# Kernel optimization log

Hardware: AMD Instinct MI355X
Metric: run time of the kernel (lower is better)

The kernel has to match this reference:

```python
import jax, jax.numpy as jnp
import numpy as np

SLOPE = 0.1
HEADS = 4
BN_EPS = 1e-5


def _gat(x, W, a_src, a_dst, mask):
    # x: (B,N,D); W: (D,D); a_src/a_dst: (H,dh); mask: (B,N,N) bool
    B, N, D = x.shape
    dh = D // HEADS
    h = (x @ W).reshape(B, N, HEADS, dh)
    s_src = jnp.einsum('bnhd,hd->bhn', h, a_src)  # score contrib of query i
    s_dst = jnp.einsum('bnhd,hd->bhn', h, a_dst)  # score contrib of key j
    e = jax.nn.leaky_relu(s_src[:, :, :, None] + s_dst[:, :, None, :], SLOPE)  # (B,H,N,N)
    e = jnp.where(mask[:, None, :, :], e, jnp.float32(-1e9))
    a = jax.nn.softmax(e, axis=-1)
    out = jnp.einsum('bhij,bjhd->bihd', a, h).reshape(B, N, D)
    return out


def setup_inputs() -> dict:
    key = jax.random.key(0)
    ks = jax.random.split(key, 20)
    B, N, F, D, Hn = 2, 2000, 64, 128, 3
    deep_dim = 3 * D
    feats = jax.random.normal(ks[0], (B, N, F), dtype=jnp.float32)
    ind = jax.random.randint(ks[1], (B, N, N), 0, 2).astype(bool)
    eye = jnp.eye(N, dtype=bool)[None]
    ind = jnp.logical_or(ind, eye)  # ensure self-loops so no all-masked row
    uni = jnp.ones((B, N, N), dtype=bool)
    s = 0.05
    return {
        'features': feats,
        'industry_mask': ind,
        'universe_mask': uni,
        # BatchNorm1d (eval mode)
        'bn_gamma': jax.random.normal(ks[2], (F,)) * s + 1.0,
        'bn_beta': jax.random.normal(ks[3], (F,)) * s,
        'bn_mean': jnp.zeros((F,), jnp.float32),
        'bn_var': jnp.ones((F,), jnp.float32),
        # encoder MLP (stored as (in,out))
        'W1': jax.random.normal(ks[4], (F, D)) * s,
        'b1': jnp.zeros((D,), jnp.float32),
        'W2': jax.random.normal(ks[5], (D, D)) * s,
        'b2': jnp.zeros((D,), jnp.float32),
        # industry GAT
        'giW': jax.random.normal(ks[6], (D, D)) * s,
        'gia_src': jax.random.normal(ks[7], (HEADS, D // HEADS)) * s,
        'gia_dst': jax.random.normal(ks[8], (HEADS, D // HEADS)) * s,
        # universe GAT
        'guW': jax.random.normal(ks[9], (D, D)) * s,
        'gua_src': jax.random.normal(ks[10], (HEADS, D // HEADS)) * s,
        'gua_dst': jax.random.normal(ks[11], (HEADS, D // HEADS)) * s,
        # per-horizon deep factor heads (Hn, deep_dim), (Hn,)
        'head_W': jax.random.normal(ks[12], (Hn, deep_dim)) * s,
        'head_b': jnp.zeros((Hn,), jnp.float32),
        # per-horizon factor attention proj (Hn, F, F), applied as x @ P_h^T
        'proj_W': jax.random.normal(ks[13], (Hn, F, F)) * s,
    }


def reference(features, industry_mask, universe_mask, bn_gamma, bn_beta, bn_mean,
              bn_var, W1, b1, W2, b2, giW, gia_src, gia_dst, guW, gua_src,
              gua_dst, head_W, head_b, proj_W):
    # --- StockContextEncoder: BN (eval) + MLP ---
    xn = (features - bn_mean) * jax.lax.rsqrt(bn_var + BN_EPS) * bn_gamma + bn_beta
    C = jax.nn.relu(xn @ W1 + b1) @ W2 + b2  # (B,N,D)
    # --- masked GATs with residual subtraction ---
    H_I = _gat(C, giW, gia_src, gia_dst, industry_mask)
    C_bar_I = C - H_I
    H_U = _gat(C_bar_I, guW, gua_src, gua_dst, universe_mask)
    C_bar_U = C_bar_I - H_U
    concat_ctx = jnp.concatenate([C, C_bar_I, C_bar_U], axis=-1)  # (B,N,3D)
    # --- per-horizon deep factor heads (vectorized over horizons) ---
    factors = jax.nn.leaky_relu(
        jnp.einsum('bnd,hd->hbn', concat_ctx, head_W) + head_b[:, None, None], SLOPE)
    # --- FactorAttention (Eq. 9-12), vectorized over horizons ---
    U = jax.nn.leaky_relu(jnp.einsum('bnm,hkm->hbnk', features, proj_W), SLOPE)
    A = jax.nn.softmax(U, axis=-1)          # (Hn,B,N,m)
    a_bar = A.mean(axis=2)                  # (Hn,B,m)
    recon = jnp.einsum('bnm,hbm->hbn', features, a_bar)
    return (C, C_bar_I, C_bar_U, H_I, H_U, factors, recon, A)
```

## Files before the change

kernel.cpp:

```cpp
#include <hip/hip_runtime.h>

#define BB 2
#define NN 2000
#define FF 64
#define DD 128
#define NH 4
#define HNZ 3
#define DEEP 384
#define NSEG 4
#define SEGSTRIDE 512
#define HTPAD 2048
#define SEGTOT (BB * NN * DD)
#define DENTOT (BB * NN * NH)

typedef __attribute__((ext_vector_type(8))) short short8;
typedef __attribute__((ext_vector_type(4))) float f32x4;
typedef unsigned short ushort_t;
typedef unsigned int uint_t;

__device__ __forceinline__ float lrelu(float x) { return x > 0.f ? x : 0.1f * x; }
__device__ __forceinline__ ushort_t f2bf(float f) {
    unsigned int u = __float_as_uint(f);
    unsigned int r = u + 0x7fffu + ((u >> 16) & 1u);
    return (ushort_t)(r >> 16);
}

__device__ __forceinline__ void proj_scores(
    const float (*Xl)[DD], const float* __restrict__ Wg,
    const float* __restrict__ a_src, const float* __restrict__ a_dst,
    ushort_t* __restrict__ hT, float* __restrict__ ssrc,
    float* __restrict__ sdst, int row0, int t)
{
    const int jq = t & 31, rg = t >> 5;
    const int r0 = 2 * rg, c0 = 4 * jq;
    float4 p0 = make_float4(0.f, 0.f, 0.f, 0.f);
    float4 p1 = make_float4(0.f, 0.f, 0.f, 0.f);
    for (int k = 0; k < DD; ++k) {
        float4 w = *(const float4*)&Wg[k * DD + c0];
        float x0 = Xl[r0][k], x1 = Xl[r0 + 1][k];
        p0.x += x0 * w.x; p0.y += x0 * w.y; p0.z += x0 * w.z; p0.w += x0 * w.w;
        p1.x += x1 * w.x; p1.y += x1 * w.y; p1.z += x1 * w.z; p1.w += x1 * w.w;
    }
    const int gr = row0 + r0;
    const int b = gr / NN, n = gr % NN;
    uint_t pk;
    pk = (uint_t)f2bf(p0.x) | ((uint_t)f2bf(p1.x) << 16);
    *(uint_t*)&hT[(b * DD + c0 + 0) * HTPAD + n] = pk;
    pk = (uint_t)f2bf(p0.y) | ((uint_t)f2bf(p1.y) << 16);
    *(uint_t*)&hT[(b * DD + c0 + 1) * HTPAD + n] = pk;
    pk = (uint_t)f2bf(p0.z) | ((uint_t)f2bf(p1.z) << 16);
    *(uint_t*)&hT[(b * DD + c0 + 2) * HTPAD + n] = pk;
    pk = (uint_t)f2bf(p0.w) | ((uint_t)f2bf(p1.w) << 16);
    *(uint_t*)&hT[(b * DD + c0 + 3) * HTPAD + n] = pk;

    float4 as4 = *(const float4*)&a_src[c0];
    float4 ad4 = *(const float4*)&a_dst[c0];
    float ps0 = p0.x * as4.x + p0.y * as4.y + p0.z * as4.z + p0.w * as4.w;
    float ps1 = p1.x * as4.x + p1.y * as4.y + p1.z * as4.z + p1.w * as4.w;
    float pd0 = p0.x * ad4.x + p0.y * ad4.y + p0.z * ad4.z + p0.w * ad4.w;
    float pd1 = p1.x * ad4.x + p1.y * ad4.y + p1.z * ad4.z + p1.w * ad4.w;
#pragma unroll
    for (int off = 1; off <= 4; off <<= 1) {
        ps0 += __shfl_xor(ps0, off);
        ps1 += __shfl_xor(ps1, off);
        pd0 += __shfl_xor(pd0, off);
        pd1 += __shfl_xor(pd1, off);
    }
    if ((jq & 7) == 0) {
        int h = jq >> 3;
        ssrc[(b * NH + h) * NN + n] = ps0;
        ssrc[(b * NH + h) * NN + n + 1] = ps1;
        sdst[(b * NH + h) * NN + n] = pd0;
        sdst[(b * NH + h) * NN + n + 1] = pd1;
    }
}

__global__ __launch_bounds__(256) void k_enc_proj(
    const float* __restrict__ feat, const float* __restrict__ gamma,
    const float* __restrict__ beta, const float* __restrict__ mean,
    const float* __restrict__ var, const float* __restrict__ W1,
    const float* __restrict__ b1, const float* __restrict__ W2,
    const float* __restrict__ b2, float* __restrict__ C,
    const float* __restrict__ Wg, const float* __restrict__ a_src,
    const float* __restrict__ a_dst, ushort_t* __restrict__ hT,
    float* __restrict__ ssrc, float* __restrict__ sdst)
{
    __shared__ float xnl[16][FF];
    __shared__ float hidl[16][DD];
    __shared__ float Cl[16][DD];
    const int row0 = blockIdx.x * 16;
    const int t = threadIdx.x;
    {
        int row = t >> 4, m0 = (t & 15) * 4;
        float4 f = *(const float4*)&feat[(row0 + row) * FF + m0];
        float4 g4 = *(const float4*)&gamma[m0];
        float4 be4 = *(const float4*)&beta[m0];
        float4 mn4 = *(const float4*)&mean[m0];
        float4 vr4 = *(const float4*)&var[m0];
        float4 xv;
        xv.x = (f.x - mn4.x) * rsqrtf(vr4.x + 1e-5f) * g4.x + be4.x;
        xv.y = (f.y - mn4.y) * rsqrtf(vr4.y + 1e-5f) * g4.y + be4.y;
        xv.z = (f.z - mn4.z) * rsqrtf(vr4.z + 1e-5f) * g4.z + be4.z;
        xv.w = (f.w - mn4.w) * rsqrtf(vr4.w + 1e-5f) * g4.w + be4.w;
        *(float4*)&xnl[row][m0] = xv;
    }
    __syncthreads();
    const int jq = t & 31, rg = t >> 5;
    const int r0 = 2 * rg, c0 = 4 * jq;
    float4 bb = *(const float4*)&b1[c0];
    float4 a0 = bb, a1 = bb;
    for (int k = 0; k < FF; ++k) {
        float4 w = *(const float4*)&W1[k * DD + c0];
        float x0 = xnl[r0][k], x1 = xnl[r0 + 1][k];
        a0.x += x0 * w.x; a0.y += x0 * w.y; a0.z += x0 * w.z; a0.w += x0 * w.w;
        a1.x += x1 * w.x; a1.y += x1 * w.y; a1.z += x1 * w.z; a1.w += x1 * w.w;
    }
    a0.x = fmaxf(a0.x, 0.f); a0.y = fmaxf(a0.y, 0.f);
    a0.z = fmaxf(a0.z, 0.f); a0.w = fmaxf(a0.w, 0.f);
    a1.x = fmaxf(a1.x, 0.f); a1.y = fmaxf(a1.y, 0.f);
    a1.z = fmaxf(a1.z, 0.f); a1.w = fmaxf(a1.w, 0.f);
    *(float4*)&hidl[r0][c0] = a0;
    *(float4*)&hidl[r0 + 1][c0] = a1;
    __syncthreads();
    bb = *(const float4*)&b2[c0];
    a0 = bb; a1 = bb;
    for (int k = 0; k < DD; ++k) {
        float4 w = *(const float4*)&W2[k * DD + c0];
        float x0 = hidl[r0][k], x1 = hidl[r0 + 1][k];
        a0.x += x0 * w.x; a0.y += x0 * w.y; a0.z += x0 * w.z; a0.w += x0 * w.w;
        a1.x += x1 * w.x; a1.y += x1 * w.y; a1.z += x1 * w.z; a1.w += x1 * w.w;
    }
    *(float4*)&C[(row0 + r0) * DD + c0] = a0;
    *(float4*)&C[(row0 + r0 + 1) * DD + c0] = a1;
    *(float4*)&Cl[r0][c0] = a0;
    *(float4*)&Cl[r0 + 1][c0] = a1;
    __syncthreads();
    proj_scores(Cl, Wg, a_src, a_dst, hT, ssrc, sdst, row0, t);
}

__global__ __launch_bounds__(256) void k_finish_proj(
    const float* __restrict__ C, const float* __restrict__ num_p,
    const float* __restrict__ den_p, float* __restrict__ H,
    float* __restrict__ Cbar, const float* __restrict__ Wg,
    const float* __restrict__ a_src, const float* __restrict__ a_dst,
    ushort_t* __restrict__ hT, float* __restrict__ ssrc,
    float* __restrict__ sdst)
{
    __shared__ float Xl[16][DD];
    __shared__ float denl[16][NH];
    const int row0 = blockIdx.x * 16;
    const int t = threadIdx.x;
    if (t < 64) {
        int rr = t >> 2, hh = t & 3;
        int gr = row0 + rr;
        float s = 0.f;
#pragma unroll
        for (int sg = 0; sg < NSEG; ++sg)
            s += den_p[sg * DENTOT + gr * NH + hh];
        denl[rr][hh] = s;
    }
    __syncthreads();
    const int jq = t & 31, rg = t >> 5;
    const int r0 = 2 * rg, c0 = 4 * jq;
    const int hh = jq >> 3;
#pragma unroll
    for (int rr = 0; rr < 2; ++rr) {
        int gr = row0 + r0 + rr;
        float4 s = make_float4(0.f, 0.f, 0.f, 0.f);
#pragma unroll
        for (int sg = 0; sg < NSEG; ++sg) {
            float4 v = *(const float4*)&num_p[sg * SEGTOT + gr * DD + c0];
            s.x += v.x; s.y += v.y; s.z += v.z; s.w += v.w;
        }
        float inv = 1.f / denl[r0 + rr][hh];
        float4 cv = *(const float4*)&C[gr * DD + c0];
        float4 Hv = make_float4(s.x * inv, s.y * inv, s.z * inv, s.w * inv);
        float4 cb = make_float4(cv.x - Hv.x, cv.y - Hv.y, cv.z - Hv.z, cv.w - Hv.w);
        *(float4*)&H[gr * DD + c0] = Hv;
        *(float4*)&Cbar[gr * DD + c0] = cb;
        *(float4*)&Xl[r0 + rr][c0] = cb;
    }
    __syncthreads();
    proj_scores(Xl, Wg, a_src, a_dst, hT, ssrc, sdst, row0, t);
}

__global__ __launch_bounds__(256) void k_gat_attn(
    const int* __restrict__ mask, const ushort_t* __restrict__ hT,
    const float* __restrict__ ssrc, const float* __restrict__ sdst,
    float* __restrict__ num_p, float* __restrict__ den_p)
{
    __shared__ float sdl[NH][SEGSTRIDE];
    const int t = threadIdx.x;
    const int iblk = blockIdx.x % 125;
    const int tmp = blockIdx.x / 125;
    const int b = tmp & 1;
    const int seg = tmp >> 1;
    const int i0 = iblk * 16;
    const int jbeg = seg * SEGSTRIDE;
    const int jlim = min(NN - jbeg, SEGSTRIDE);

    const int h = t >> 6;
    const int l = t & 63;
    const int il = l & 15;
    const int g = l >> 4;

    for (int jj = l; jj < jlim; jj += 64)
        sdl[h][jj] = sdst[(b * NH + h) * NN + jbeg + jj];
    __syncthreads();

    const float sS = ssrc[(b * NH + h) * NN + i0 + il];
    const int* mrow = mask + (long)b * NN * NN + (long)(i0 + il) * NN + jbeg;
    const ushort_t* hrow0 = hT + ((b * DD + 32 * h + il) * HTPAD + jbeg);
    const ushort_t* hrow1 = hrow0 + 16 * HTPAD;

    f32x4 acc0 = {0.f, 0.f, 0.f, 0.f};
    f32x4 acc1 = {0.f, 0.f, 0.f, 0.f};
    float den_acc = 0.f;

    for (int jc = 0; jc < SEGSTRIDE; jc += 32) {
        const int jloc = jc + 8 * g;
        int4 m0 = make_int4(0, 0, 0, 0), m1 = make_int4(0, 0, 0, 0);
        if (jloc < jlim)     m0 = *(const int4*)(mrow + jloc);
        if (jloc + 4 < jlim) m1 = *(const int4*)(mrow + jloc + 4);
        float4 s0 = *(const float4*)&sdl[h][jloc];
        float4 s1 = *(const float4*)&sdl[h][jloc + 4];
        float w[8];
        w[0] = m0.x ? __expf(lrelu(sS + s0.x)) : 0.f;
        w[1] = m0.y ? __expf(lrelu(sS + s0.y)) : 0.f;
        w[2] = m0.z ? __expf(lrelu(sS + s0.z)) : 0.f;
        w[3] = m0.w ? __expf(lrelu(sS + s0.w)) : 0.f;
        w[4] = m1.x ? __expf(lrelu(sS + s1.x)) : 0.f;
        w[5] = m1.y ? __expf(lrelu(sS + s1.y)) : 0.f;
        w[6] = m1.z ? __expf(lrelu(sS + s1.z)) : 0.f;
        w[7] = m1.w ? __expf(lrelu(sS + s1.w)) : 0.f;
        short8 af;
#pragma unroll
        for (int e = 0; e < 8; ++e) {
            den_acc += w[e];
            af[e] = (short)f2bf(w[e]);
        }
        short8 bf0 = *(const short8*)(hrow0 + jloc);
        short8 bf1 = *(const short8*)(hrow1 + jloc);
        acc0 = __builtin_amdgcn_mfma_f32_16x16x32_bf16(af, bf0, acc0, 0, 0, 0);
        acc1 = __builtin_amdgcn_mfma_f32_16x16x32_bf16(af, bf1, acc1, 0, 0, 0);
    }

    den_acc += __shfl_xor(den_acc, 16);
    den_acc += __shfl_xor(den_acc, 32);
    if (l < 16)
        den_p[seg * DENTOT + (b * NN + i0 + l) * NH + h] = den_acc;

    const long segbase = (long)seg * SEGTOT;
#pragma unroll
    for (int r = 0; r < 4; ++r) {
        long base = segbase + ((long)b * NN + i0 + 4 * g + r) * DD + 32 * h + il;
        num_p[base] = acc0[r];
        num_p[base + 16] = acc1[r];
    }
}

__global__ __launch_bounds__(256) void k_finish(
    const float* __restrict__ X, const float* __restrict__ num_p,
    const float* __restrict__ den_p, float* __restrict__ H,
    float* __restrict__ Cbar)
{
    int idx = blockIdx.x * 256 + threadIdx.x;
    if (idx >= BB * NN * DD / 4) return;
    int row = idx >> 5;
    int d4 = idx & 31;
    float den = 0.f;
#pragma unroll
    for (int sg = 0; sg < NSEG; ++sg)
        den += den_p[sg * DENTOT + row * NH + (d4 >> 3)];
    float4 s = make_float4(0.f, 0.f, 0.f, 0.f);
#pragma unroll
    for (int sg = 0; sg < NSEG; ++sg) {
        float4 v = ((const float4*)(num_p + (long)sg * SEGTOT))[idx];
        s.x += v.x; s.y += v.y; s.z += v.z; s.w += v.w;
    }
    float inv = 1.f / den;
    float4 xv = ((const float4*)X)[idx];
    float4 ho = make_float4(s.x * inv, s.y * inv, s.z * inv, s.w * inv);
    ((float4*)H)[idx] = ho;
    ((float4*)Cbar)[idx] =
        make_float4(xv.x - ho.x, xv.y - ho.y, xv.z - ho.z, xv.w - ho.w);
}

__global__ __launch_bounds__(256) void k_factor_attn(
    const float* __restrict__ feat, const float* __restrict__ proj_W,
    float* __restrict__ A, float* __restrict__ abar)
{
    __shared__ float Pt[FF][FF + 1];
    __shared__ float fl[8][FF];
    __shared__ float abpart[4][FF];
    const int hb = blockIdx.x / 250;
    const int n_base = (blockIdx.x % 250) * 8;
    const int h = hb >> 1, b = hb & 1;
    const int t = threadIdx.x;
    for (int idx = t; idx < FF * FF; idx += 256) {
        int k = idx >> 6, m = idx & 63;
        Pt[m][k] = proj_W[(h * FF + k) * FF + m];
    }
    for (int idx = t; idx < 8 * FF / 4; idx += 256) {
        int r = idx >> 4, m0 = (idx & 15) * 4;
        *(float4*)&fl[r][m0] =
            *(const float4*)&feat[(b * NN + n_base + r) * FF + m0];
    }
    __syncthreads();
    const int ns = t >> 6, k = t & 63;
    float u0 = 0.f, u1 = 0.f;
    for (int m = 0; m < FF; ++m) {
        float p = Pt[m][k];
        u0 += fl[ns][m] * p;
        u1 += fl[ns + 4][m] * p;
    }
    u0 = lrelu(u0); u1 = lrelu(u1);
    float mx0 = u0, mx1 = u1;
#pragma unroll
    for (int off = 32; off; off >>= 1) {
        mx0 = fmaxf(mx0, __shfl_xor(mx0, off));
        mx1 = fmaxf(mx1, __shfl_xor(mx1, off));
    }
    float e0 = __expf(u0 - mx0), e1 = __expf(u1 - mx1);
    float sm0 = e0, sm1 = e1;
#pragma unroll
    for (int off = 32; off; off >>= 1) {
        sm0 += __shfl_xor(sm0, off);
        sm1 += __shfl_xor(sm1, off);
    }
    float a0 = e0 / sm0, a1 = e1 / sm1;
    A[((h * BB + b) * NN + n_base + ns) * FF + k] = a0;
    A[((h * BB + b) * NN + n_base + ns + 4) * FF + k] = a1;
    abpart[ns][k] = a0 + a1;
    __syncthreads();
    if (t < FF) {
        float s = abpart[0][t] + abpart[1][t] + abpart[2][t] + abpart[3][t];
        atomicAdd(&abar[(h * BB + b) * FF + t], s);
    }
}

__global__ __launch_bounds__(256) void k_factors_recon(
    const float* __restrict__ C, const float* __restrict__ CbI,
    const float* __restrict__ CbU, const float* __restrict__ head_W,
    const float* __restrict__ head_b, const float* __restrict__ feat,
    const float* __restrict__ abar, float* __restrict__ factors,
    float* __restrict__ recon)
{
    int out = blockIdx.x * 4 + (threadIdx.x >> 6);
    int l = threadIdx.x & 63;
    if (out >= HNZ * BB * NN) return;
    int h = out / (BB * NN);
    int rn = out % (BB * NN);
    const float* w = head_W + h * DEEP;
    float acc = C[rn * DD + l] * w[l] + C[rn * DD + l + 64] * w[l + 64]
              + CbI[rn * DD + l] * w[128 + l] + CbI[rn * DD + l + 64] * w[192 + l]
              + CbU[rn * DD + l] * w[256 + l] + CbU[rn * DD + l + 64] * w[320 + l];
    float racc = feat[rn * FF + l] * abar[(h * BB + rn / NN) * FF + l];
#pragma unroll
    for (int off = 32; off; off >>= 1) {
        acc += __shfl_xor(acc, off);
        racc += __shfl_xor(racc, off);
    }
    if (l == 0) {
        factors[out] = lrelu(acc + head_b[h]);
        recon[out] = racc * (1.f / NN);
    }
}

extern "C" void kernel_launch(void* const* d_in, const int* in_sizes, int n_in,
                              void* d_out, int out_size, void* d_ws, size_t ws_size,
                              hipStream_t stream)
{
    const float* feat     = (const float*)d_in[0];
    const int*   ind_mask = (const int*)d_in[1];
    const int*   uni_mask = (const int*)d_in[2];
    const float* bn_gamma = (const float*)d_in[3];
    const float* bn_beta  = (const float*)d_in[4];
    const float* bn_mean  = (const float*)d_in[5];
    const float* bn_var   = (const float*)d_in[6];
    const float* W1 = (const float*)d_in[7];
    const float* b1 = (const float*)d_in[8];
    const float* W2 = (const float*)d_in[9];
    const float* b2 = (const float*)d_in[10];
    const float* giW = (const float*)d_in[11];
    const float* gia_src = (const float*)d_in[12];
    const float* gia_dst = (const float*)d_in[13];
    const float* guW = (const float*)d_in[14];
    const float* gua_src = (const float*)d_in[15];
    const float* gua_dst = (const float*)d_in[16];
    const float* head_W = (const float*)d_in[17];
    const float* head_b = (const float*)d_in[18];
    const float* proj_W = (const float*)d_in[19];

    float* out = (float*)d_out;
    float* C       = out;
    float* CbI     = out + 512000;
    float* CbU     = out + 1024000;
    float* H_I     = out + 1536000;
    float* H_U     = out + 2048000;
    float* factors = out + 2560000;
    float* recon   = out + 2572000;
    float* A       = out + 2584000;

    float* ws = (float*)d_ws;
    ushort_t* hT = (ushort_t*)ws;
    float* ssrc  = ws + 262400;
    float* sdst  = ws + 278400;
    float* den_p = ws + 294400;
    float* num_p = ws + 358400;
    float* abar  = ws + 2406400;

    hipMemsetAsync(abar, 0, HNZ * BB * FF * sizeof(float), stream);

    k_factor_attn<<<HNZ * BB * 250, 256, 0, stream>>>(feat, proj_W, A, abar);

    k_enc_proj<<<BB * NN / 16, 256, 0, stream>>>(
        feat, bn_gamma, bn_beta, bn_mean, bn_var, W1, b1, W2, b2, C,
        giW, gia_src, gia_dst, hT, ssrc, sdst);
    k_gat_attn<<<NSEG * BB * 125, 256, 0, stream>>>(
        ind_mask, hT, ssrc, sdst, num_p, den_p);
    k_finish_proj<<<BB * NN / 16, 256, 0, stream>>>(
        C, num_p, den_p, H_I, CbI, guW, gua_src, gua_dst, hT, ssrc, sdst);
    k_gat_attn<<<NSEG * BB * 125, 256, 0, stream>>>(
        uni_mask, hT, ssrc, sdst, num_p, den_p);
    k_finish<<<500, 256, 0, stream>>>(CbI, num_p, den_p, H_U, CbU);

    k_factors_recon<<<3000, 256, 0, stream>>>(
        C, CbI, CbU, head_W, head_b, feat, abar, factors, recon);
}
```

Baseline: 239.2 us.

## Fuse final GAT finish with factor heads and streamline attention exp path

The final GAT finish kernel and the factor/reconstruction head kernel are merged into one kernel that keeps the concatenated context for 8 rows in shared memory. This removes a launch and the re-read of C, CbI and CbU from global memory. The attention inner loop now pre-scales scores by log2(e) so it can call the raw exp2 instruction directly, uses fmax for leaky ReLU, and packs bf16 with the hardware convert instruction instead of manual rounding. It also splits the denominator accumulation into two chains. Rounding may differ slightly from the old manual round-to-nearest-even conversion.

```diff
diff --git a/kernel.cpp b/kernel.cpp
--- a/kernel.cpp
+++ b/kernel.cpp
@@ -12,6 +12,7 @@
 #define HTPAD 2048
 #define SEGTOT (BB * NN * DD)
 #define DENTOT (BB * NN * NH)
+#define LOG2E 1.44269504f
 
 typedef __attribute__((ext_vector_type(8))) short short8;
 typedef __attribute__((ext_vector_type(4))) float f32x4;
@@ -68,10 +69,10 @@
     }
     if ((jq & 7) == 0) {
         int h = jq >> 3;
-        ssrc[(b * NH + h) * NN + n] = ps0;
-        ssrc[(b * NH + h) * NN + n + 1] = ps1;
-        sdst[(b * NH + h) * NN + n] = pd0;
-        sdst[(b * NH + h) * NN + n + 1] = pd1;
+        ssrc[(b * NH + h) * NN + n] = ps0 * LOG2E;
+        ssrc[(b * NH + h) * NN + n + 1] = ps1 * LOG2E;
+        sdst[(b * NH + h) * NN + n] = pd0 * LOG2E;
+        sdst[(b * NH + h) * NN + n + 1] = pd1 * LOG2E;
     }
 }
 
@@ -215,7 +216,7 @@
 
     f32x4 acc0 = {0.f, 0.f, 0.f, 0.f};
     f32x4 acc1 = {0.f, 0.f, 0.f, 0.f};
-    float den_acc = 0.f;
+    float den0 = 0.f, den1 = 0.f;
 
     for (int jc = 0; jc < SEGSTRIDE; jc += 32) {
         const int jloc = jc + 8 * g;
@@ -224,27 +225,34 @@
         if (jloc + 4 < jlim) m1 = *(const int4*)(mrow + jloc + 4);
         float4 s0 = *(const float4*)&sdl[h][jloc];
         float4 s1 = *(const float4*)&sdl[h][jloc + 4];
-        float w[8];
-        w[0] = m0.x ? __expf(lrelu(sS + s0.x)) : 0.f;
-        w[1] = m0.y ? __expf(lrelu(sS + s0.y)) : 0.f;
-        w[2] = m0.z ? __expf(lrelu(sS + s0.z)) : 0.f;
-        w[3] = m0.w ? __expf(lrelu(sS + s0.w)) : 0.f;
-        w[4] = m1.x ? __expf(lrelu(sS + s1.x)) : 0.f;
-        w[5] = m1.y ? __expf(lrelu(sS + s1.y)) : 0.f;
-        w[6] = m1.z ? __expf(lrelu(sS + s1.z)) : 0.f;
-        w[7] = m1.w ? __expf(lrelu(sS + s1.w)) : 0.f;
-        short8 af;
-#pragma unroll
-        for (int e = 0; e < 8; ++e) {
-            den_acc += w[e];
-            af[e] = (short)f2bf(w[e]);
+        float w0, w1, w2, w3, w4, w5, w6, w7;
+        {
+            float x, e;
+#define SCORE(SRC, MM, OUT)                                        \
+            x = sS + SRC;                                          \
+            x = fmaxf(x, 0.1f * x);                                \
+            asm("v_exp_f32 %0, %1" : "=v"(e) : "v"(x));            \
+            OUT = MM ? e : 0.f;
+            SCORE(s0.x, m0.x, w0) SCORE(s0.y, m0.y, w1)
+            SCORE(s0.z, m0.z, w2) SCORE(s0.w, m0.w, w3)
+            SCORE(s1.x, m1.x, w4) SCORE(s1.y, m1.y, w5)
+            SCORE(s1.z, m1.z, w6) SCORE(s1.w, m1.w, w7)
+#undef SCORE
         }
+        den0 += (w0 + w1) + (w2 + w3);
+        den1 += (w4 + w5) + (w6 + w7);
+        union { uint_t u[4]; short8 s8; } pk;
+        asm("v_cvt_pk_bf16_f32 %0, %1, %2" : "=v"(pk.u[0]) : "v"(w0), "v"(w1));
+        asm("v_cvt_pk_bf16_f32 %0, %1, %2" : "=v"(pk.u[1]) : "v"(w2), "v"(w3));
+        asm("v_cvt_pk_bf16_f32 %0, %1, %2" : "=v"(pk.u[2]) : "v"(w4), "v"(w5));
+        asm("v_cvt_pk_bf16_f32 %0, %1, %2" : "=v"(pk.u[3]) : "v"(w6), "v"(w7));
         short8 bf0 = *(const short8*)(hrow0 + jloc);
         short8 bf1 = *(const short8*)(hrow1 + jloc);
-        acc0 = __builtin_amdgcn_mfma_f32_16x16x32_bf16(af, bf0, acc0, 0, 0, 0);
-        acc1 = __builtin_amdgcn_mfma_f32_16x16x32_bf16(af, bf1, acc1, 0, 0, 0);
-    }
-
+        acc0 = __builtin_amdgcn_mfma_f32_16x16x32_bf16(pk.s8, bf0, acc0, 0, 0, 0);
+        acc1 = __builtin_amdgcn_mfma_f32_16x16x32_bf16(pk.s8, bf1, acc1, 0, 0, 0);
+    }
+
+    float den_acc = den0 + den1;
     den_acc += __shfl_xor(den_acc, 16);
     den_acc += __shfl_xor(den_acc, 32);
     if (l < 16)
@@ -259,31 +267,71 @@
     }
 }
 
-__global__ __launch_bounds__(256) void k_finish(
-    const float* __restrict__ X, const float* __restrict__ num_p,
-    const float* __restrict__ den_p, float* __restrict__ H,
-    float* __restrict__ Cbar)
-{
-    int idx = blockIdx.x * 256 + threadIdx.x;
-    if (idx >= BB * NN * DD / 4) return;
-    int row = idx >> 5;
-    int d4 = idx & 31;
-    float den = 0.f;
-#pragma unroll
-    for (int sg = 0; sg < NSEG; ++sg)
-        den += den_p[sg * DENTOT + row * NH + (d4 >> 3)];
-    float4 s = make_float4(0.f, 0.f, 0.f, 0.f);
-#pragma unroll
-    for (int sg = 0; sg < NSEG; ++sg) {
-        float4 v = ((const float4*)(num_p + (long)sg * SEGTOT))[idx];
-        s.x += v.x; s.y += v.y; s.z += v.z; s.w += v.w;
-    }
-    float inv = 1.f / den;
-    float4 xv = ((const float4*)X)[idx];
-    float4 ho = make_float4(s.x * inv, s.y * inv, s.z * inv, s.w * inv);
-    ((float4*)H)[idx] = ho;
-    ((float4*)Cbar)[idx] =
-        make_float4(xv.x - ho.x, xv.y - ho.y, xv.z - ho.z, xv.w - ho.w);
+__global__ __launch_bounds__(256) void k_finish_factors(
+    const float* __restrict__ C, const float* __restrict__ CbI,
+    const float* __restrict__ num_p, const float* __restrict__ den_p,
+    float* __restrict__ H, float* __restrict__ CbU,
+    const float* __restrict__ head_W, const float* __restrict__ head_b,
+    const float* __restrict__ feat, const float* __restrict__ abar,
+    float* __restrict__ factors, float* __restrict__ recon)
+{
+    __shared__ float ctx[8][DEEP];
+    __shared__ float denl[8][NH];
+    const int row0 = blockIdx.x * 8;
+    const int t = threadIdx.x;
+    if (t < 32) {
+        int rr = t >> 2, hh = t & 3;
+        float s = 0.f;
+#pragma unroll
+        for (int sg = 0; sg < NSEG; ++sg)
+            s += den_p[sg * DENTOT + (row0 + rr) * NH + hh];
+        denl[rr][hh] = s;
+    }
+    __syncthreads();
+    {
+        const int r = t >> 5, c0 = (t & 31) * 4;
+        const int gr = row0 + r;
+        float4 s = make_float4(0.f, 0.f, 0.f, 0.f);
+#pragma unroll
+        for (int sg = 0; sg < NSEG; ++sg) {
+            float4 v = *(const float4*)&num_p[sg * SEGTOT + gr * DD + c0];
+            s.x += v.x; s.y += v.y; s.z += v.z; s.w += v.w;
+        }
+        float inv = 1.f / denl[r][(t & 31) >> 3];
+        float4 ci = *(const float4*)&CbI[gr * DD + c0];
+        float4 cv = *(const float4*)&C[gr * DD + c0];
+        float4 Hv = make_float4(s.x * inv, s.y * inv, s.z * inv, s.w * inv);
+        float4 cu = make_float4(ci.x - Hv.x, ci.y - Hv.y, ci.z - Hv.z, ci.w - Hv.w);
+        *(float4*)&H[gr * DD + c0] = Hv;
+        *(float4*)&CbU[gr * DD + c0] = cu;
+        *(float4*)&ctx[r][c0] = cv;
+        *(float4*)&ctx[r][DD + c0] = ci;
+        *(float4*)&ctx[r][2 * DD + c0] = cu;
+    }
+    __syncthreads();
+    const int wv = t >> 6, l = t & 63, sub = l >> 5, ll = l & 31;
+    const int lr = wv * 2 + sub;
+    const int grr = row0 + lr;
+    const int b = grr / NN;
+#pragma unroll
+    for (int h = 0; h < HNZ; ++h) {
+        const float* w = head_W + h * DEEP;
+        float a = 0.f;
+#pragma unroll
+        for (int d = 0; d < DEEP; d += 32) a += ctx[lr][d + ll] * w[d + ll];
+        const float* ab = abar + (h * BB + b) * FF;
+        float rc = feat[grr * FF + ll] * ab[ll]
+                 + feat[grr * FF + ll + 32] * ab[ll + 32];
+#pragma unroll
+        for (int off = 16; off; off >>= 1) {
+            a += __shfl_xor(a, off);
+            rc += __shfl_xor(rc, off);
+        }
+        if (ll == 0) {
+            factors[h * (BB * NN) + grr] = lrelu(a + head_b[h]);
+            recon[h * (BB * NN) + grr] = rc * (1.f / NN);
+        }
+    }
 }
 
 __global__ __launch_bounds__(256) void k_factor_attn(
@@ -336,34 +384,6 @@
     if (t < FF) {
         float s = abpart[0][t] + abpart[1][t] + abpart[2][t] + abpart[3][t];
         atomicAdd(&abar[(h * BB + b) * FF + t], s);
-    }
-}
-
-__global__ __launch_bounds__(256) void k_factors_recon(
-    const float* __restrict__ C, const float* __restrict__ CbI,
-    const float* __restrict__ CbU, const float* __restrict__ head_W,
-    const float* __restrict__ head_b, const float* __restrict__ feat,
-    const float* __restrict__ abar, float* __restrict__ factors,
-    float* __restrict__ recon)
-{
-    int out = blockIdx.x * 4 + (threadIdx.x >> 6);
-    int l = threadIdx.x & 63;
-    if (out >= HNZ * BB * NN) return;
-    int h = out / (BB * NN);
-    int rn = out % (BB * NN);
-    const float* w = head_W + h * DEEP;
-    float acc = C[rn * DD + l] * w[l] + C[rn * DD + l + 64] * w[l + 64]
-              + CbI[rn * DD + l] * w[128 + l] + CbI[rn * DD + l + 64] * w[192 + l]
-              + CbU[rn * DD + l] * w[256 + l] + CbU[rn * DD + l + 64] * w[320 + l];
-    float racc = feat[rn * FF + l] * abar[(h * BB + rn / NN) * FF + l];
-#pragma unroll
-    for (int off = 32; off; off >>= 1) {
-        acc += __shfl_xor(acc, off);
-        racc += __shfl_xor(racc, off);
-    }
-    if (l == 0) {
-        factors[out] = lrelu(acc + head_b[h]);
-        recon[out] = racc * (1.f / NN);
     }
 }
 
@@ -423,8 +443,7 @@
         C, num_p, den_p, H_I, CbI, guW, gua_src, gua_dst, hT, ssrc, sdst);
     k_gat_attn<<<NSEG * BB * 125, 256, 0, stream>>>(
         uni_mask, hT, ssrc, sdst, num_p, den_p);
-    k_finish<<<500, 256, 0, stream>>>(CbI, num_p, den_p, H_U, CbU);
-
-    k_factors_recon<<<3000, 256, 0, stream>>>(
-        C, CbI, CbU, head_W, head_b, feat, abar, factors, recon);
-}
+    k_finish_factors<<<500, 256, 0, stream>>>(
+        C, CbI, num_p, den_p, H_U, CbU,
+        head_W, head_b, feat, abar, factors, recon);
+}
```

New measurement: 236.5 us. Within noise of the previous version (-1.1%).
